# Kernel optimization log

Hardware: AMD Instinct MI355X
Metric: run time of the kernel (lower is better)

The kernel has to match this reference:

```python
import jax, jax.numpy as jnp
import numpy as np

B, T, D = 1, 4096, 2048
H, G, K = 16, 4, 128   # query heads, kv heads, head_dim
R = H // G             # n_rep = 4
EPS = 1e-6
SCALE = K ** -0.5


def rms_norm(x, scale):
    var = jnp.mean(x.astype(jnp.float32) ** 2, axis=-1, keepdims=True)
    normed = x * jax.lax.rsqrt(var + EPS)
    return (scale * normed).astype(x.dtype)


def apply_rope(x_BTHK, sin_BTK, cos_BTK):
    half = x_BTHK.shape[-1] // 2
    x1, x2 = x_BTHK[..., :half], x_BTHK[..., half:]
    s = sin_BTK[:, :, None, :]
    c = cos_BTK[:, :, None, :]
    return jnp.concatenate([x1 * c - x2 * s, x2 * c + x1 * s], axis=-1).astype(x_BTHK.dtype)


def setup_inputs() -> dict:
    key = jax.random.key(0)
    ks = jax.random.split(key, 8)
    hidden = jax.random.normal(ks[0], (B, T, D), dtype=jnp.float32)
    # rope angles
    inv_freq = 1.0 / (10000.0 ** (jnp.arange(0, K, 2, dtype=jnp.float32) / K))  # [K/2]
    pos = jnp.arange(T, dtype=jnp.float32)
    ang = pos[:, None] * inv_freq[None, :]          # [T, K/2]
    sin = jnp.broadcast_to(jnp.sin(ang)[None], (B, T, K // 2))
    cos = jnp.broadcast_to(jnp.cos(ang)[None], (B, T, K // 2))
    mask = jnp.broadcast_to(jnp.tril(jnp.ones((T, T), dtype=bool))[None], (B, T, T))
    std = D ** -0.5
    Wq = jax.random.normal(ks[1], (D, H * K), dtype=jnp.float32) * std
    Wk = jax.random.normal(ks[2], (D, G * K), dtype=jnp.float32) * std
    Wv = jax.random.normal(ks[3], (D, G * K), dtype=jnp.float32) * std
    Wo = jax.random.normal(ks[4], (H * K, D), dtype=jnp.float32) * ((H * K) ** -0.5)
    q_scale = jnp.ones((K,), dtype=jnp.float32)
    k_scale = jnp.ones((K,), dtype=jnp.float32)
    return {"hidden_BTD": hidden, "sin_BTK": sin, "cos_BTK": cos, "mask": mask,
            "Wq": Wq, "Wk": Wk, "Wv": Wv, "Wo": Wo,
            "q_scale": q_scale, "k_scale": k_scale}


def reference(hidden_BTD, sin_BTK, cos_BTK, mask, Wq, Wk, Wv, Wo, q_scale, k_scale):
    q = rms_norm((hidden_BTD @ Wq).reshape(B, T, H, K), q_scale)
    k = rms_norm((hidden_BTD @ Wk).reshape(B, T, G, K), k_scale)
    v = (hidden_BTD @ Wv).reshape(B, T, G, K)
    q = apply_rope(q, sin_BTK, cos_BTK)
    k = apply_rope(k, sin_BTK, cos_BTK)
    q_BTGRK = q.reshape(B, T, G, R, K)
    logits = jnp.einsum('BTGRK,BSGK->BTSGR', q_BTGRK, k) * SCALE
    neg = float(jnp.finfo(logits.dtype).min)
    logits = jnp.where(mask[:, :, :, None, None], logits, neg)
    weights = jax.nn.softmax(logits.astype(jnp.float32), axis=2).astype(logits.dtype)
    attn = jnp.einsum('BTSGR,BSGK->BTGRK', weights, v)
    return attn.reshape(B, T, H * K) @ Wo
```

## Files before the change

### kernel.cpp

```cpp
#include <hip/hip_runtime.h>
#include <hip/hip_bf16.h>
#include <stdint.h>

#define T_SEQ 4096
#define KVB 64
#define BM 128
#define BN 128
#define BK 64
#define SCL2 (0.08838834764831845f * 1.44269504088896340f)

typedef unsigned short u16;
typedef __attribute__((ext_vector_type(8))) short s16x8;
typedef __attribute__((ext_vector_type(4))) short s16x4;
typedef __attribute__((ext_vector_type(4))) float f32x4;

__device__ __forceinline__ u16 f2bf(float f) {
  union { float f; unsigned u; } a; a.f = f;
  unsigned r = a.u + 0x7fffu + ((a.u >> 16) & 1u);
  return (u16)(r >> 16);
}
__device__ __forceinline__ float bf2f(u16 b) {
  union { unsigned u; float f; } a; a.u = ((unsigned)b) << 16;
  return a.f;
}
__device__ __forceinline__ unsigned cvtpk(float lo, float hi) {
  unsigned r;
  asm volatile("v_cvt_pk_bf16_f32 %0, %1, %2" : "=v"(r) : "v"(lo), "v"(hi));
  return r;
}

__device__ __forceinline__ void gl_lds16(const void* g, void* l) {
  __builtin_amdgcn_global_load_lds((const __attribute__((address_space(1))) void*)g,
                                   (__attribute__((address_space(3))) void*)l, 16, 0, 0);
}

__global__ __launch_bounds__(256) void k_prep(const float* __restrict__ hidden, u16* __restrict__ Xb,
                                              const float* __restrict__ Wq, const float* __restrict__ Wk,
                                              const float* __restrict__ Wv, const float* __restrict__ Wo,
                                              u16* __restrict__ Bqkv, u16* __restrict__ Wot) {
  __shared__ float tile[32][33];
  int bid = blockIdx.x;
  if (bid < 4096) {
    int i = (bid * 256 + threadIdx.x) * 8;
    const float4* p = (const float4*)(hidden + i);
    float4 a = p[0], b = p[1];
    s16x8 o;
    o[0] = (short)f2bf(a.x); o[1] = (short)f2bf(a.y); o[2] = (short)f2bf(a.z); o[3] = (short)f2bf(a.w);
    o[4] = (short)f2bf(b.x); o[5] = (short)f2bf(b.y); o[6] = (short)f2bf(b.z); o[7] = (short)f2bf(b.w);
    *(s16x8*)(Xb + i) = o;
    return;
  }
  const float* in;
  u16* out;
  int R, C, l;
  if (bid < 8192)       { in = Wq; out = Bqkv;              R = 2048; C = 2048; l = bid - 4096; }
  else if (bid < 9216)  { in = Wk; out = Bqkv + 2048 * 2048; R = 2048; C = 512;  l = bid - 8192; }
  else if (bid < 10240) { in = Wv; out = Bqkv + 2560 * 2048; R = 2048; C = 512;  l = bid - 9216; }
  else                  { in = Wo; out = Wot;               R = 2048; C = 2048; l = bid - 10240; }
  int nbx = C >> 5;
  int bx = l % nbx, by = l / nbx;
  int c0 = bx * 32, r0 = by * 32;
  int tx = threadIdx.x & 31, ty = threadIdx.x >> 5;
#pragma unroll
  for (int k = 0; k < 4; k++) tile[ty + 8 * k][tx] = in[(size_t)(r0 + ty + 8 * k) * C + c0 + tx];
  __syncthreads();
#pragma unroll
  for (int k = 0; k < 4; k++) out[(size_t)(c0 + ty + 8 * k) * R + r0 + tx] = f2bf(tile[tx][ty + 8 * k]);
}

__global__ __launch_bounds__(256, 2) void k_gemm(const u16* __restrict__ A, const u16* __restrict__ Bt,
                                                 u16* __restrict__ Cq, u16* __restrict__ Ck, u16* __restrict__ Cvt,
                                                 float* __restrict__ Cf, int M, int N, int Kd, int mode) {
  __shared__ u16 SM[BM * BK + BN * BK];
  u16* As = SM;
  u16* Bs = SM + BM * BK;
  int tid = threadIdx.x, lane = tid & 63, w = tid >> 6;
  int g = lane >> 4, r16 = lane & 15;
  int lidb = blockIdx.y * gridDim.x + blockIdx.x;
  int per = (gridDim.x * gridDim.y) >> 3;
  int nid = (lidb & 7) * per + (lidb >> 3);
  int ty = nid / gridDim.x;
  int m0 = ty * BM, n0 = (nid - ty * gridDim.x) * BN;
  int wr = w >> 1, wc = w & 1;
  f32x4 acc[4][4] = {};

  for (int kt = 0; kt < Kd; kt += BK) {
#pragma unroll
    for (int i = 0; i < 4; i++) {
      int idx = i * 256 + tid;
      int row = idx >> 3, c = idx & 7;
      int cs = c ^ (row & 7);
      gl_lds16(A + (size_t)(m0 + row) * Kd + kt + cs * 8, As + (i * 256 + w * 64) * 8);
    }
#pragma unroll
    for (int i = 0; i < 4; i++) {
      int idx = i * 256 + tid;
      int row = idx >> 3, c = idx & 7;
      int cs = c ^ (row & 7);
      gl_lds16(Bt + (size_t)(n0 + row) * Kd + kt + cs * 8, Bs + (i * 256 + w * 64) * 8);
    }
    __syncthreads();
#pragma unroll
    for (int kk = 0; kk < 2; kk++) {
      s16x8 af[4], bfr[4];
#pragma unroll
      for (int mi = 0; mi < 4; mi++) {
        int row = wr * 64 + mi * 16 + r16;
        af[mi] = *(const s16x8*)(As + row * 64 + (((kk * 4 + g) ^ (row & 7)) * 8));
      }
#pragma unroll
      for (int ni = 0; ni < 4; ni++) {
        int row = wc * 64 + ni * 16 + r16;
        bfr[ni] = *(const s16x8*)(Bs + row * 64 + (((kk * 4 + g) ^ (row & 7)) * 8));
      }
#pragma unroll
      for (int mi = 0; mi < 4; mi++)
#pragma unroll
        for (int ni = 0; ni < 4; ni++)
          acc[mi][ni] = __builtin_amdgcn_mfma_f32_16x16x32_bf16(af[mi], bfr[ni], acc[mi][ni], 0, 0, 0);
    }
    __syncthreads();
  }

#pragma unroll
  for (int mi = 0; mi < 4; mi++) {
    int rowb = m0 + wr * 64 + mi * 16 + g * 4;
#pragma unroll
    for (int ni = 0; ni < 4; ni++) {
      int ncol0 = n0 + wc * 64 + ni * 16;
      int col = ncol0 + r16;
      if (mode == 0) {
        if (ncol0 < 2048) {
#pragma unroll
          for (int j = 0; j < 4; j++) Cq[(size_t)(rowb + j) * 2048 + col] = f2bf(acc[mi][ni][j]);
        } else if (ncol0 < 2560) {
#pragma unroll
          for (int j = 0; j < 4; j++) Ck[(size_t)(rowb + j) * 512 + (col - 2048)] = f2bf(acc[mi][ni][j]);
        } else {
          s16x4 pk;
#pragma unroll
          for (int j = 0; j < 4; j++) pk[j] = (short)f2bf(acc[mi][ni][j]);
          *(s16x4*)(Cvt + (size_t)(col - 2560) * T_SEQ + rowb) = pk;
        }
      } else {
#pragma unroll
        for (int j = 0; j < 4; j++) Cf[(size_t)(rowb + j) * N + col] = acc[mi][ni][j];
      }
    }
  }
}

__global__ __launch_bounds__(256) void k_normrope(u16* __restrict__ Q, u16* __restrict__ Kc,
                                                  const float* __restrict__ sinT, const float* __restrict__ cosT,
                                                  const float* __restrict__ qsc, const float* __restrict__ ksc) {
  int t = blockIdx.x;
  int w = threadIdx.x >> 6, lane = threadIdx.x & 63;
  int unit = blockIdx.y * 4 + w;
  u16* base;
  const float* sc;
  float fold;
  if (unit < 16) { base = Q + (size_t)t * 2048 + unit * 128; sc = qsc; fold = SCL2; }
  else { base = Kc + (size_t)t * 512 + (unit - 16) * 128; sc = ksc; fold = 1.0f; }
  float x1 = bf2f(base[lane]), x2 = bf2f(base[lane + 64]);
  float ss = x1 * x1 + x2 * x2;
#pragma unroll
  for (int off = 32; off >= 1; off >>= 1) ss += __shfl_xor(ss, off);
  float rinv = rsqrtf(ss * (1.0f / 128.0f) + 1e-6f);
  float n1 = x1 * rinv * sc[lane], n2 = x2 * rinv * sc[lane + 64];
  float s = sinT[t * 64 + lane], c = cosT[t * 64 + lane];
  base[lane] = f2bf((n1 * c - n2 * s) * fold);
  base[lane + 64] = f2bf((n2 * c + n1 * s) * fold);
}

__global__ __launch_bounds__(256, 2) void k_attn(const u16* __restrict__ Q, const u16* __restrict__ Kc,
                                                 const u16* __restrict__ Vt, u16* __restrict__ O) {
  __shared__ __align__(16) char SMc[73728];
  int tid = threadIdx.x, lane = tid & 63, w = tid >> 6;
  int g = lane >> 4, r16 = lane & 15;
  int qs = w >> 1, ks = w & 1;

  int bid = blockIdx.x;
  int xcd = bid & 7;
  int lid = bid >> 3;
  int h = xcd * 2 + (lid & 1);
  int qb = 63 - (lid >> 1);
  int gh = h >> 2;
  int q0 = qb * 64;
  int qwv = q0 + qs * 32;
  int nt = qb + 1;

  s16x8 qf[2][4];
#pragma unroll
  for (int qc = 0; qc < 2; qc++)
#pragma unroll
    for (int dc = 0; dc < 4; dc++)
      qf[qc][dc] = *(const s16x8*)(Q + (size_t)(qwv + qc * 16 + r16) * 2048 + h * 128 + dc * 32 + g * 8);

  auto STAGE = [&](int bb, int tt) {
    int kv0 = tt * KVB;
    u16* Kb = (u16*)(SMc + bb * 16384);
    u16* Vb = (u16*)(SMc + 32768 + bb * 16384);
#pragma unroll
    for (int i = 0; i < 4; i++) {
      int idx = i * 256 + tid;
      int row = idx >> 4, cc = idx & 15;
      int cs = cc ^ (row & 7);
      gl_lds16(Kc + (size_t)(kv0 + row) * 512 + gh * 128 + cs * 8, Kb + (i * 256 + w * 64) * 8);
    }
#pragma unroll
    for (int i = 0; i < 4; i++) {
      int idx = i * 256 + tid;
      int row = idx >> 3, cc = idx & 7;
      int cs = cc ^ (row & 7);
      gl_lds16(Vt + (size_t)(gh * 128 + row) * T_SEQ + kv0 + cs * 8, Vb + (i * 256 + w * 64) * 8);
    }
  };

  f32x4 acc[2][8] = {};
  float mrun[2] = {-3.0e38f, -3.0e38f};
  float lrun[2] = {0.0f, 0.0f};

  STAGE(0, 0);
  __syncthreads();

  for (int t = 0; t < nt; ++t) {
    int kv0 = t * KVB;
    int bb = t & 1;
    STAGE(bb ^ 1, (t + 1 < nt) ? t + 1 : 0);

    int kvw = kv0 + ks * 32;
    if (kvw <= qwv + 31) {
      u16* Kb = (u16*)(SMc + bb * 16384);
      u16* Vb = (u16*)(SMc + 32768 + bb * 16384);
      char* Pwb = SMc + 65536 + w * 2048;

      f32x4 sv[2][2] = {};
      __builtin_amdgcn_s_setprio(1);
#pragma unroll
      for (int kc = 0; kc < 2; kc++) {
        int krow = ks * 32 + kc * 16 + r16;
#pragma unroll
        for (int dc = 0; dc < 4; dc++) {
          s16x8 kf = *(const s16x8*)((u16*)Kb + krow * 128 + (((dc * 4 + g) ^ (krow & 7)) * 8));
          sv[0][kc] = __builtin_amdgcn_mfma_f32_16x16x32_bf16(kf, qf[0][dc], sv[0][kc], 0, 0, 0);
          sv[1][kc] = __builtin_amdgcn_mfma_f32_16x16x32_bf16(kf, qf[1][dc], sv[1][kc], 0, 0, 0);
        }
      }
      __builtin_amdgcn_s_setprio(0);

#pragma unroll
      for (int qc = 0; qc < 2; qc++) {
        int qg = qwv + qc * 16 + r16;
        bool needmask = (kvw + 31) > (qwv + qc * 16);
        if (needmask) {
#pragma unroll
          for (int kc = 0; kc < 2; kc++)
#pragma unroll
            for (int j2 = 0; j2 < 4; j2++)
              if (kvw + kc * 16 + g * 4 + j2 > qg) sv[qc][kc][j2] = -3.0e38f;
        }
        float mt = sv[qc][0][0];
#pragma unroll
        for (int kc = 0; kc < 2; kc++)
#pragma unroll
          for (int j2 = 0; j2 < 4; j2++) mt = fmaxf(mt, sv[qc][kc][j2]);
        mt = fmaxf(mt, __shfl_xor(mt, 16));
        mt = fmaxf(mt, __shfl_xor(mt, 32));
        if (__any(mt > mrun[qc] + 8.0f)) {
          float mnew = fmaxf(mrun[qc], mt);
          float al = exp2f(mrun[qc] - mnew);
          mrun[qc] = mnew;
          lrun[qc] *= al;
#pragma unroll
          for (int df = 0; df < 8; df++) acc[qc][df] = acc[qc][df] * al;
        }
        float rs = 0.0f;
#pragma unroll
        for (int kc = 0; kc < 2; kc++) {
          float p0 = exp2f(sv[qc][kc][0] - mrun[qc]);
          float p1 = exp2f(sv[qc][kc][1] - mrun[qc]);
          float p2 = exp2f(sv[qc][kc][2] - mrun[qc]);
          float p3 = exp2f(sv[qc][kc][3] - mrun[qc]);
          rs += (p0 + p1) + (p2 + p3);
          uint2 pk;
          pk.x = cvtpk(p0, p1);
          pk.y = cvtpk(p2, p3);
          int unit = ((qc << 2) | (kc << 1) | (g >> 1)) ^ (r16 & 7);
          *(uint2*)(Pwb + r16 * 128 + unit * 16 + (g & 1) * 8) = pk;
        }
        rs += __shfl_xor(rs, 16);
        rs += __shfl_xor(rs, 32);
        lrun[qc] += rs;
      }

      __builtin_amdgcn_s_setprio(1);
      s16x8 pf0 = *(const s16x8*)(Pwb + r16 * 128 + (((0 * 4 + g) ^ (r16 & 7)) * 16));
      s16x8 pf1 = *(const s16x8*)(Pwb + r16 * 128 + (((1 * 4 + g) ^ (r16 & 7)) * 16));
#pragma unroll
      for (int df = 0; df < 8; df++) {
        int vrow = df * 16 + r16;
        s16x8 vf = *(const s16x8*)((u16*)Vb + vrow * 64 + (((ks * 4 + g) ^ (vrow & 7)) * 8));
        acc[0][df] = __builtin_amdgcn_mfma_f32_16x16x32_bf16(vf, pf0, acc[0][df], 0, 0, 0);
        acc[1][df] = __builtin_amdgcn_mfma_f32_16x16x32_bf16(vf, pf1, acc[1][df], 0, 0, 0);
      }
      __builtin_amdgcn_s_setprio(0);
    }
    __syncthreads();
  }

  float* ml = (float*)(SMc + 65536);
  if (g < 2) {
    float mv = g ? mrun[1] : mrun[0];
    float lv = g ? lrun[1] : lrun[0];
    int mi = ((w * 2 + g) * 16 + r16) * 2;
    ml[mi] = mv;
    ml[mi + 1] = lv;
  }
  __syncthreads();
  int pw = w ^ 1;
  float scale[2];
#pragma unroll
  for (int qc = 0; qc < 2; qc++) {
    float pm = ml[((pw * 2 + qc) * 16 + r16) * 2];
    float pl = ml[((pw * 2 + qc) * 16 + r16) * 2 + 1];
    float ms = fmaxf(mrun[qc], pm);
    float aS = exp2f(mrun[qc] - ms);
    float aP = exp2f(pm - ms);
    float ls = lrun[qc] * aS + pl * aP;
    scale[qc] = aS / ls;
  }
  char* obw = SMc + qs * 16384 + ks * 32768;
#pragma unroll
  for (int qc = 0; qc < 2; qc++)
#pragma unroll
    for (int df = 0; df < 8; df++) {
      f32x4 v = acc[qc][df] * scale[qc];
      int r = qc * 16 + r16;
      int u = df * 4 + g;
      int up = u ^ ((r & 7) << 2);
      *(f32x4*)(obw + r * 512 + up * 16) = v;
    }
  __syncthreads();
#pragma unroll
  for (int it = 0; it < 8; it++) {
    int item = it * 256 + tid;
    int qs2 = item >> 10, rem = item & 1023;
    int r = rem >> 5, u = rem & 31;
    int up = u ^ ((r & 7) << 2);
    f32x4 a = *(const f32x4*)(SMc + qs2 * 16384 + r * 512 + up * 16);
    f32x4 b = *(const f32x4*)(SMc + 32768 + qs2 * 16384 + r * 512 + up * 16);
    f32x4 sSum = a + b;
    uint2 pk;
    pk.x = cvtpk(sSum[0], sSum[1]);
    pk.y = cvtpk(sSum[2], sSum[3]);
    *(uint2*)(O + (size_t)(q0 + qs2 * 32 + r) * 2048 + h * 128 + u * 4) = pk;
  }
}

extern "C" void kernel_launch(void* const* d_in, const int* in_sizes, int n_in,
                              void* d_out, int out_size, void* d_ws, size_t ws_size,
                              hipStream_t stream) {
  const float* hidden = (const float*)d_in[0];
  const float* sinT = (const float*)d_in[1];
  const float* cosT = (const float*)d_in[2];
  const float* Wq = (const float*)d_in[4];
  const float* Wk = (const float*)d_in[5];
  const float* Wv = (const float*)d_in[6];
  const float* Wo = (const float*)d_in[7];
  const float* qsc = (const float*)d_in[8];
  const float* ksc = (const float*)d_in[9];
  float* out = (float*)d_out;

  char* ws = (char*)d_ws;
  u16* Xb   = (u16*)(ws + 0);
  u16* Bqkv = (u16*)(ws + 16777216);
  u16* Wot  = (u16*)(ws + 29360128);
  u16* Qraw = (u16*)(ws + 37748736);
  u16* Kraw = (u16*)(ws + 54525952);
  u16* Vt   = (u16*)(ws + 58720256);
  u16* Oat  = (u16*)(ws + 62914560);

  k_prep<<<dim3(14336), dim3(256), 0, stream>>>(hidden, Xb, Wq, Wk, Wv, Wo, Bqkv, Wot);
  k_gemm<<<dim3(24, 32), dim3(256), 0, stream>>>(Xb, Bqkv, Qraw, Kraw, Vt, (float*)nullptr,
                                                 4096, 3072, 2048, 0);
  k_normrope<<<dim3(4096, 5), dim3(256), 0, stream>>>(Qraw, Kraw, sinT, cosT, qsc, ksc);
  k_attn<<<dim3(1024), dim3(256), 0, stream>>>(Qraw, Kraw, Vt, Oat);
  k_gemm<<<dim3(16, 32), dim3(256), 0, stream>>>(Oat, Wot, (u16*)nullptr, (u16*)nullptr, (u16*)nullptr,
                                                 out, 4096, 2048, 2048, 1);
}
```

Measured before the change: 258.5 us.

## Single-buffer V and shrink LDS to fit three attention blocks per CU

V staging drops from double to single buffering. The next V tile is loaded only after the PV MFMAs finish, and an extra barrier is added per iteration. The P scratch buffer is halved, and the final two-warp combine now has one warp write to LDS and the partner warp read and add directly. Together this cuts shared memory from 72KB to 52KB and raises launch bounds to 3 blocks per CU. The cost is less overlap of V loads with compute and more barriers per KV tile.

```diff
diff --git a/kernel.cpp b/kernel.cpp
--- a/kernel.cpp
+++ b/kernel.cpp
@@ -172,9 +172,9 @@
   base[lane + 64] = f2bf((n2 * c + n1 * s) * fold);
 }
 
-__global__ __launch_bounds__(256, 2) void k_attn(const u16* __restrict__ Q, const u16* __restrict__ Kc,
+__global__ __launch_bounds__(256, 3) void k_attn(const u16* __restrict__ Q, const u16* __restrict__ Kc,
                                                  const u16* __restrict__ Vt, u16* __restrict__ O) {
-  __shared__ __align__(16) char SMc[73728];
+  __shared__ __align__(16) char SMc[53248];
   int tid = threadIdx.x, lane = tid & 63, w = tid >> 6;
   int g = lane >> 4, r16 = lane & 15;
   int qs = w >> 1, ks = w & 1;
@@ -196,10 +196,9 @@
     for (int dc = 0; dc < 4; dc++)
       qf[qc][dc] = *(const s16x8*)(Q + (size_t)(qwv + qc * 16 + r16) * 2048 + h * 128 + dc * 32 + g * 8);
 
-  auto STAGE = [&](int bb, int tt) {
+  auto STAGE_K = [&](int bb, int tt) {
     int kv0 = tt * KVB;
     u16* Kb = (u16*)(SMc + bb * 16384);
-    u16* Vb = (u16*)(SMc + 32768 + bb * 16384);
 #pragma unroll
     for (int i = 0; i < 4; i++) {
       int idx = i * 256 + tid;
@@ -207,6 +206,10 @@
       int cs = cc ^ (row & 7);
       gl_lds16(Kc + (size_t)(kv0 + row) * 512 + gh * 128 + cs * 8, Kb + (i * 256 + w * 64) * 8);
     }
+  };
+  auto STAGE_V = [&](int tt) {
+    int kv0 = tt * KVB;
+    u16* Vb = (u16*)(SMc + 32768);
 #pragma unroll
     for (int i = 0; i < 4; i++) {
       int idx = i * 256 + tid;
@@ -220,19 +223,21 @@
   float mrun[2] = {-3.0e38f, -3.0e38f};
   float lrun[2] = {0.0f, 0.0f};
 
-  STAGE(0, 0);
+  STAGE_K(0, 0);
+  STAGE_V(0);
   __syncthreads();
 
   for (int t = 0; t < nt; ++t) {
     int kv0 = t * KVB;
     int bb = t & 1;
-    STAGE(bb ^ 1, (t + 1 < nt) ? t + 1 : 0);
+    if (t + 1 < nt) STAGE_K(bb ^ 1, t + 1);
 
     int kvw = kv0 + ks * 32;
-    if (kvw <= qwv + 31) {
+    bool live = (kvw <= qwv + 31);
+    s16x8 pfr[2];
+    if (live) {
       u16* Kb = (u16*)(SMc + bb * 16384);
-      u16* Vb = (u16*)(SMc + 32768 + bb * 16384);
-      char* Pwb = SMc + 65536 + w * 2048;
+      char* Pwb = SMc + 49152 + w * 1024;
 
       f32x4 sv[2][2] = {};
       __builtin_amdgcn_s_setprio(1);
@@ -285,37 +290,42 @@
           uint2 pk;
           pk.x = cvtpk(p0, p1);
           pk.y = cvtpk(p2, p3);
-          int unit = ((qc << 2) | (kc << 1) | (g >> 1)) ^ (r16 & 7);
-          *(uint2*)(Pwb + r16 * 128 + unit * 16 + (g & 1) * 8) = pk;
+          int slotW = (kc * 2 + (g >> 1)) ^ (r16 & 3);
+          *(uint2*)(Pwb + r16 * 64 + slotW * 16 + (g & 1) * 8) = pk;
         }
         rs += __shfl_xor(rs, 16);
         rs += __shfl_xor(rs, 32);
         lrun[qc] += rs;
-      }
-
+        pfr[qc] = *(const s16x8*)(Pwb + r16 * 64 + ((g ^ (r16 & 3)) * 16));
+      }
+    }
+    __syncthreads();
+
+    if (live) {
+      u16* Vb = (u16*)(SMc + 32768);
       __builtin_amdgcn_s_setprio(1);
-      s16x8 pf0 = *(const s16x8*)(Pwb + r16 * 128 + (((0 * 4 + g) ^ (r16 & 7)) * 16));
-      s16x8 pf1 = *(const s16x8*)(Pwb + r16 * 128 + (((1 * 4 + g) ^ (r16 & 7)) * 16));
 #pragma unroll
       for (int df = 0; df < 8; df++) {
         int vrow = df * 16 + r16;
         s16x8 vf = *(const s16x8*)((u16*)Vb + vrow * 64 + (((ks * 4 + g) ^ (vrow & 7)) * 8));
-        acc[0][df] = __builtin_amdgcn_mfma_f32_16x16x32_bf16(vf, pf0, acc[0][df], 0, 0, 0);
-        acc[1][df] = __builtin_amdgcn_mfma_f32_16x16x32_bf16(vf, pf1, acc[1][df], 0, 0, 0);
+        acc[0][df] = __builtin_amdgcn_mfma_f32_16x16x32_bf16(vf, pfr[0], acc[0][df], 0, 0, 0);
+        acc[1][df] = __builtin_amdgcn_mfma_f32_16x16x32_bf16(vf, pfr[1], acc[1][df], 0, 0, 0);
       }
       __builtin_amdgcn_s_setprio(0);
     }
     __syncthreads();
-  }
-
-  float* ml = (float*)(SMc + 65536);
-  if (g < 2) {
-    float mv = g ? mrun[1] : mrun[0];
-    float lv = g ? lrun[1] : lrun[0];
-    int mi = ((w * 2 + g) * 16 + r16) * 2;
-    ml[mi] = mv;
-    ml[mi + 1] = lv;
-  }
+
+    if (t + 1 < nt) STAGE_V(t + 1);
+  }
+
+  float* ml = (float*)(SMc + 32768);
+#pragma unroll
+  for (int qc = 0; qc < 2; qc++)
+    if (g == 0) {
+      int mi = ((w * 2 + qc) * 16 + r16) * 2;
+      ml[mi] = mrun[qc];
+      ml[mi + 1] = lrun[qc];
+    }
   __syncthreads();
   int pw = w ^ 1;
   float scale[2];
@@ -329,31 +339,28 @@
     float ls = lrun[qc] * aS + pl * aP;
     scale[qc] = aS / ls;
   }
-  char* obw = SMc + qs * 16384 + ks * 32768;
-#pragma unroll
-  for (int qc = 0; qc < 2; qc++)
-#pragma unroll
-    for (int df = 0; df < 8; df++) {
-      f32x4 v = acc[qc][df] * scale[qc];
-      int r = qc * 16 + r16;
-      int u = df * 4 + g;
-      int up = u ^ ((r & 7) << 2);
-      *(f32x4*)(obw + r * 512 + up * 16) = v;
-    }
+  if (ks == 0) {
+#pragma unroll
+    for (int qc = 0; qc < 2; qc++)
+#pragma unroll
+      for (int df = 0; df < 8; df++) {
+        f32x4 v = acc[qc][df] * scale[qc];
+        *(f32x4*)(SMc + qs * 16384 + (qc * 16 + r16) * 512 + (((df * 4 + g) ^ (r16 & 7)) * 16)) = v;
+      }
+  }
   __syncthreads();
-#pragma unroll
-  for (int it = 0; it < 8; it++) {
-    int item = it * 256 + tid;
-    int qs2 = item >> 10, rem = item & 1023;
-    int r = rem >> 5, u = rem & 31;
-    int up = u ^ ((r & 7) << 2);
-    f32x4 a = *(const f32x4*)(SMc + qs2 * 16384 + r * 512 + up * 16);
-    f32x4 b = *(const f32x4*)(SMc + 32768 + qs2 * 16384 + r * 512 + up * 16);
-    f32x4 sSum = a + b;
-    uint2 pk;
-    pk.x = cvtpk(sSum[0], sSum[1]);
-    pk.y = cvtpk(sSum[2], sSum[3]);
-    *(uint2*)(O + (size_t)(q0 + qs2 * 32 + r) * 2048 + h * 128 + u * 4) = pk;
+  if (ks == 1) {
+#pragma unroll
+    for (int qc = 0; qc < 2; qc++)
+#pragma unroll
+      for (int df = 0; df < 8; df++) {
+        f32x4 p = *(const f32x4*)(SMc + qs * 16384 + (qc * 16 + r16) * 512 + (((df * 4 + g) ^ (r16 & 7)) * 16));
+        f32x4 o = p + acc[qc][df] * scale[qc];
+        uint2 pk;
+        pk.x = cvtpk(o[0], o[1]);
+        pk.y = cvtpk(o[2], o[3]);
+        *(uint2*)(O + (size_t)(q0 + qs * 32 + qc * 16 + r16) * 2048 + h * 128 + df * 16 + g * 4) = pk;
+      }
   }
 }
 
```

Measured after the change: 288.8 us. 11.7% more time.
